# Kernel tuning notes

Hardware: AMD Instinct MI355X
Metric: run time of the kernel (lower is better)

Reference implementation:

```python
import jax, jax.numpy as jnp
import numpy as np

N_NODES = 50000
N_EDGES = 500000
IN_DIM = 128
HIDDEN = 32
HEADS = 8
OUT_DIM = HIDDEN * HEADS  # 256
NEG_SLOPE = 0.2


def setup_inputs() -> dict:
    key = jax.random.key(0)
    ks = jax.random.split(key, 10)
    s = lambda fan: 1.0 / np.sqrt(fan)
    x = jax.random.normal(ks[0], (N_NODES, IN_DIM), dtype=jnp.float32)
    edge_index = jax.random.randint(ks[1], (2, N_EDGES), 0, N_NODES, dtype=jnp.int32)
    W1 = jax.random.normal(ks[2], (IN_DIM, HEADS * HIDDEN), jnp.float32) * s(IN_DIM)
    a_src1 = jax.random.normal(ks[3], (HEADS, HIDDEN), jnp.float32) * s(HIDDEN)
    a_dst1 = jax.random.normal(ks[4], (HEADS, HIDDEN), jnp.float32) * s(HIDDEN)
    b1 = jnp.zeros((HEADS * HIDDEN,), jnp.float32)
    W2 = jax.random.normal(ks[5], (OUT_DIM, OUT_DIM), jnp.float32) * s(OUT_DIM)
    a_src2 = jax.random.normal(ks[6], (1, OUT_DIM), jnp.float32) * s(OUT_DIM)
    a_dst2 = jax.random.normal(ks[7], (1, OUT_DIM), jnp.float32) * s(OUT_DIM)
    b2 = jnp.zeros((OUT_DIM,), jnp.float32)
    return {"x": x, "edge_index": edge_index, "W1": W1, "a_src1": a_src1,
            "a_dst1": a_dst1, "b1": b1, "W2": W2, "a_src2": a_src2,
            "a_dst2": a_dst2, "b2": b2}


def _gat_layer(x, src, dst, W, a_src, a_dst, b, heads, ch, concat):
    N = x.shape[0]
    h = (x @ W).reshape(N, heads, ch)                      # [N,H,C]
    e_src = jnp.sum(h * a_src[None], axis=-1)              # [N,H]
    e_dst = jnp.sum(h * a_dst[None], axis=-1)              # [N,H]
    e = jax.nn.leaky_relu(e_src[src] + e_dst[dst], NEG_SLOPE)  # [E,H]
    # softmax over incoming edges of each destination node
    m = jax.ops.segment_max(e, dst, num_segments=N)        # [N,H]
    e = jnp.exp(e - m[dst])
    denom = jax.ops.segment_sum(e, dst, num_segments=N)    # [N,H]
    alpha = e / (denom[dst] + 1e-16)                       # [E,H]
    msg = h[src] * alpha[:, :, None]                       # [E,H,C]
    out = jax.ops.segment_sum(msg, dst, num_segments=N)    # [N,H,C]
    out = out.reshape(N, heads * ch) if concat else out.mean(axis=1)
    return out + b


def reference(x, edge_index, W1, a_src1, a_dst1, b1, W2, a_src2, a_dst2, b2):
    N = x.shape[0]
    # add self loops (PyG GATConv default)
    loops = jnp.arange(N, dtype=edge_index.dtype)
    src = jnp.concatenate([edge_index[0], loops])
    dst = jnp.concatenate([edge_index[1], loops])
    # dropout is identity in eval mode
    h = _gat_layer(x, src, dst, W1, a_src1, a_dst1, b1, HEADS, HIDDEN, True)
    h = jax.nn.elu(h)
    out = _gat_layer(h, src, dst, W2, a_src2, a_dst2, b2, 1, OUT_DIM, False)
    return out
```

## Files before the change

kernel.cpp:

```cpp
#include <hip/hip_runtime.h>
#include <math.h>

#define N_NODES 50000
#define E_ORIG  500000
#define E_TOT   550000
#define NB      196

typedef _Float16 half8 __attribute__((ext_vector_type(8)));
typedef _Float16 half4 __attribute__((ext_vector_type(4)));
typedef float    v4f   __attribute__((ext_vector_type(4)));

__global__ void k_prepw(const float* __restrict__ W1, const float* __restrict__ W2,
                        const float* __restrict__ as2, const float* __restrict__ ad2,
                        const int* __restrict__ ei,
                        _Float16* __restrict__ w1t, _Float16* __restrict__ w2t,
                        float* __restrict__ vs2, float* __restrict__ vd2,
                        int* __restrict__ deg) {
    int i = blockIdx.x * blockDim.x + threadIdx.x;
    if (i < E_TOT) {
        int d = (i < E_ORIG) ? ei[E_ORIG + i] : (i - E_ORIG);
        atomicAdd(&deg[d], 1);
        return;
    }
    int j = i - E_TOT;
    if (j < 128 * 256) {
        int k = j >> 8, c = j & 255;
        w1t[(size_t)c * 128 + k] = (_Float16)W1[j];
        return;
    }
    j -= 128 * 256;
    if (j < 256 * 256) {
        int k = j >> 8, c = j & 255;
        w2t[(size_t)c * 256 + k] = (_Float16)W2[j];
        return;
    }
    j -= 256 * 256;
    if (j < 256) {
        float s = 0.f, d = 0.f;
        for (int c = 0; c < 256; c++) {
            float w = W2[(size_t)j * 256 + c];
            s += w * as2[c];
            d += w * ad2[c];
        }
        vs2[j] = s;
        vd2[j] = d;
    }
}

__global__ __launch_bounds__(256) void k_blocksum(const int* __restrict__ deg,
                                                  int* __restrict__ bsum) {
    int t = threadIdx.x;
    int i = blockIdx.x * 256 + t;
    int v = (i < N_NODES) ? deg[i] : 0;
#pragma unroll
    for (int mk = 1; mk < 64; mk <<= 1) v += __shfl_xor(v, mk, 64);
    __shared__ int ws[4];
    if ((t & 63) == 0) ws[t >> 6] = v;
    __syncthreads();
    if (t == 0) bsum[blockIdx.x] = ws[0] + ws[1] + ws[2] + ws[3];
}

__global__ __launch_bounds__(256) void k_scanbsum(const int* __restrict__ bsum,
                                                  int* __restrict__ boff) {
    __shared__ int s[256];
    int t = threadIdx.x;
    int v = (t < NB) ? bsum[t] : 0;
    s[t] = v;
    __syncthreads();
    for (int o = 1; o < 256; o <<= 1) {
        int x = (t >= o) ? s[t - o] : 0;
        __syncthreads();
        s[t] += x;
        __syncthreads();
    }
    if (t <= NB) boff[t] = (t == 0) ? 0 : s[t - 1];
}

__global__ __launch_bounds__(256) void k_offsets(const int* __restrict__ deg,
                                                 const int* __restrict__ boff,
                                                 int* __restrict__ offsets,
                                                 int* __restrict__ cur) {
    __shared__ int s[256];
    int t = threadIdx.x;
    int i = blockIdx.x * 256 + t;
    int v = (i < N_NODES) ? deg[i] : 0;
    s[t] = v;
    __syncthreads();
    for (int o = 1; o < 256; o <<= 1) {
        int x = (t >= o) ? s[t - o] : 0;
        __syncthreads();
        s[t] += x;
        __syncthreads();
    }
    int off = boff[blockIdx.x] + s[t] - v;
    if (i <= N_NODES) {
        offsets[i] = off;
        if (i < N_NODES) cur[i] = off;
    }
}

__global__ void k_scatter(const int* __restrict__ ei, int* __restrict__ cur,
                          int* __restrict__ csr_src) {
    int e = blockIdx.x * blockDim.x + threadIdx.x;
    if (e >= E_TOT) return;
    int s, d;
    if (e < E_ORIG) { s = ei[e]; d = ei[E_ORIG + e]; }
    else            { s = e - E_ORIG; d = s; }
    int slot = atomicAdd(&cur[d], 1);
    csr_src[slot] = s;
}

__global__ __launch_bounds__(256) void k_gemm1(
    const float* __restrict__ X, const _Float16* __restrict__ Bt,
    const float* __restrict__ a_s, const float* __restrict__ a_d,
    _Float16* __restrict__ H, float* __restrict__ es, float* __restrict__ ed) {
    int t = threadIdx.x, w = t >> 6, lane = t & 63;
    int quad = lane >> 4, l16 = lane & 15;
    int row0 = blockIdx.x * 32;
    int colbase = w * 64;

    v4f acc[2][4];
#pragma unroll
    for (int i = 0; i < 2; i++)
#pragma unroll
        for (int j = 0; j < 4; j++) acc[i][j] = (v4f){0.f, 0.f, 0.f, 0.f};

    int r0 = row0 + l16;      if (r0 >= N_NODES) r0 = N_NODES - 1;
    int r1 = row0 + 16 + l16; if (r1 >= N_NODES) r1 = N_NODES - 1;
    const float4* a0p = (const float4*)(X + (size_t)r0 * 128) + quad * 2;
    const float4* a1p = (const float4*)(X + (size_t)r1 * 128) + quad * 2;
    const half8* bp[4];
#pragma unroll
    for (int ct = 0; ct < 4; ct++)
        bp[ct] = (const half8*)(Bt + (size_t)(colbase + ct * 16 + l16) * 128 + quad * 8);

#pragma unroll
    for (int kc = 0; kc < 4; kc++) {
        float4 f0 = a0p[kc * 8], f1 = a0p[kc * 8 + 1];
        float4 f2 = a1p[kc * 8], f3 = a1p[kc * 8 + 1];
        half8 av0 = (half8){(_Float16)f0.x, (_Float16)f0.y, (_Float16)f0.z, (_Float16)f0.w,
                            (_Float16)f1.x, (_Float16)f1.y, (_Float16)f1.z, (_Float16)f1.w};
        half8 av1 = (half8){(_Float16)f2.x, (_Float16)f2.y, (_Float16)f2.z, (_Float16)f2.w,
                            (_Float16)f3.x, (_Float16)f3.y, (_Float16)f3.z, (_Float16)f3.w};
#pragma unroll
        for (int ct = 0; ct < 4; ct++) {
            half8 bv = bp[ct][kc * 4];
            acc[0][ct] = __builtin_amdgcn_mfma_f32_16x16x32_f16(av0, bv, acc[0][ct], 0, 0, 0);
            acc[1][ct] = __builtin_amdgcn_mfma_f32_16x16x32_f16(av1, bv, acc[1][ct], 0, 0, 0);
        }
    }

    float asv[4], adv[4];
#pragma unroll
    for (int ct = 0; ct < 4; ct++) {
        asv[ct] = a_s[colbase + ct * 16 + l16];
        adv[ct] = a_d[colbase + ct * 16 + l16];
    }
#pragma unroll
    for (int rt = 0; rt < 2; rt++) {
#pragma unroll
        for (int hp = 0; hp < 2; hp++) {
#pragma unroll
            for (int reg = 0; reg < 4; reg++) {
                float ps = acc[rt][2 * hp][reg] * asv[2 * hp] +
                           acc[rt][2 * hp + 1][reg] * asv[2 * hp + 1];
                float pd = acc[rt][2 * hp][reg] * adv[2 * hp] +
                           acc[rt][2 * hp + 1][reg] * adv[2 * hp + 1];
#pragma unroll
                for (int mk = 1; mk < 16; mk <<= 1) {
                    ps += __shfl_xor(ps, mk, 64);
                    pd += __shfl_xor(pd, mk, 64);
                }
                if (l16 == 0) {
                    int row = row0 + rt * 16 + quad * 4 + reg;
                    if (row < N_NODES) {
                        int head = w * 2 + hp;
                        es[(size_t)row * 8 + head] = ps;
                        ed[(size_t)row * 8 + head] = pd;
                    }
                }
            }
        }
    }

    __shared__ _Float16 SH[16][264];
#pragma unroll
    for (int rt = 0; rt < 2; rt++) {
        if (rt) __syncthreads();
#pragma unroll
        for (int ct = 0; ct < 4; ct++)
#pragma unroll
            for (int reg = 0; reg < 4; reg++)
                SH[quad * 4 + reg][colbase + ct * 16 + l16] = (_Float16)acc[rt][ct][reg];
        __syncthreads();
#pragma unroll
        for (int j = 0; j < 2; j++) {
            int c = j * 256 + t;
            int row = c >> 5, col8 = c & 31;
            int gr = row0 + rt * 16 + row;
            if (gr < N_NODES)
                *(half8*)(H + (size_t)gr * 256 + col8 * 8) = *(const half8*)&SH[row][col8 * 8];
        }
    }
}

__global__ __launch_bounds__(256) void k_gemm2(
    const _Float16* __restrict__ A, const _Float16* __restrict__ Bt,
    const float* __restrict__ bias, float* __restrict__ OUT) {
    int t = threadIdx.x, w = t >> 6, lane = t & 63;
    int quad = lane >> 4, l16 = lane & 15;
    int row0 = blockIdx.x * 32;
    int colbase = w * 64;

    v4f acc[2][4];
#pragma unroll
    for (int i = 0; i < 2; i++)
#pragma unroll
        for (int j = 0; j < 4; j++) acc[i][j] = (v4f){0.f, 0.f, 0.f, 0.f};

    int r0 = row0 + l16;      if (r0 >= N_NODES) r0 = N_NODES - 1;
    int r1 = row0 + 16 + l16; if (r1 >= N_NODES) r1 = N_NODES - 1;
    const half8* a0 = (const half8*)(A + (size_t)r0 * 256 + quad * 8);
    const half8* a1 = (const half8*)(A + (size_t)r1 * 256 + quad * 8);
    const half8* bp[4];
#pragma unroll
    for (int ct = 0; ct < 4; ct++)
        bp[ct] = (const half8*)(Bt + (size_t)(colbase + ct * 16 + l16) * 256 + quad * 8);

#pragma unroll
    for (int kc = 0; kc < 8; kc++) {
        half8 av0 = a0[kc * 4];
        half8 av1 = a1[kc * 4];
#pragma unroll
        for (int ct = 0; ct < 4; ct++) {
            half8 bv = bp[ct][kc * 4];
            acc[0][ct] = __builtin_amdgcn_mfma_f32_16x16x32_f16(av0, bv, acc[0][ct], 0, 0, 0);
            acc[1][ct] = __builtin_amdgcn_mfma_f32_16x16x32_f16(av1, bv, acc[1][ct], 0, 0, 0);
        }
    }

    __shared__ float SF[16][260];
#pragma unroll
    for (int rt = 0; rt < 2; rt++) {
        if (rt) __syncthreads();
#pragma unroll
        for (int ct = 0; ct < 4; ct++)
#pragma unroll
            for (int reg = 0; reg < 4; reg++)
                SF[quad * 4 + reg][colbase + ct * 16 + l16] = acc[rt][ct][reg];
        __syncthreads();
#pragma unroll
        for (int j = 0; j < 4; j++) {
            int c = j * 256 + t;
            int row = c >> 6, c4 = c & 63;
            int gr = row0 + rt * 16 + row;
            if (gr < N_NODES) {
                float4 v = *(const float4*)&SF[row][c4 * 4];
                float4 bb = ((const float4*)bias)[c4];
                float4 o = make_float4(v.x + bb.x, v.y + bb.y, v.z + bb.z, v.w + bb.w);
                *(float4*)(OUT + (size_t)gr * 256 + c4 * 4) = o;
            }
        }
    }
}

__global__ __launch_bounds__(256) void k_agg1(
    const _Float16* __restrict__ H1, const float* __restrict__ es,
    const float* __restrict__ ed, const int* __restrict__ offsets,
    const int* __restrict__ csr_src, const float* __restrict__ b1,
    const float* __restrict__ vs2, const float* __restrict__ vd2,
    _Float16* __restrict__ out1, float* __restrict__ es2,
    float* __restrict__ ed2) {
    int t = threadIdx.x, w = t >> 6, lane = t & 63;
    int n = blockIdx.x * 4 + w;
    int hB = lane >> 3;
    int beg = offsets[n];
    int deg = offsets[n + 1] - beg;
    float edl = ed[(size_t)n * 8 + hB];

    const char* __restrict__ Hb  = (const char*)H1 + lane * 8;
    const char* __restrict__ esb = (const char*)es + hB * 4;
    float a0 = 0.f, a1 = 0.f, a2 = 0.f, a3 = 0.f, den = 0.f;

    for (int base = 0; base < deg; base += 64) {
        int rem = deg - base; if (rem > 64) rem = 64;
        int idx = beg + base + lane;
        if (idx >= E_TOT) idx = E_TOT - 1;
        int sreg = csr_src[idx];
        int i = 0;
        for (; i + 3 < rem; i += 4) {
            int s0 = __shfl(sreg, i), s1 = __shfl(sreg, i + 1);
            int s2 = __shfl(sreg, i + 2), s3 = __shfl(sreg, i + 3);
            float l0 = *(const float*)(esb + ((unsigned)s0 << 5)) + edl;
            float l1 = *(const float*)(esb + ((unsigned)s1 << 5)) + edl;
            float l2 = *(const float*)(esb + ((unsigned)s2 << 5)) + edl;
            float l3 = *(const float*)(esb + ((unsigned)s3 << 5)) + edl;
            half4 h0 = *(const half4*)(Hb + ((unsigned)s0 << 9));
            half4 h1 = *(const half4*)(Hb + ((unsigned)s1 << 9));
            half4 h2 = *(const half4*)(Hb + ((unsigned)s2 << 9));
            half4 h3 = *(const half4*)(Hb + ((unsigned)s3 << 9));
            l0 = l0 > 0.f ? l0 : 0.2f * l0;
            l1 = l1 > 0.f ? l1 : 0.2f * l1;
            l2 = l2 > 0.f ? l2 : 0.2f * l2;
            l3 = l3 > 0.f ? l3 : 0.2f * l3;
            float w0 = __expf(l0), w1 = __expf(l1);
            float w2 = __expf(l2), w3 = __expf(l3);
            a0 += w0 * (float)h0[0]; a1 += w0 * (float)h0[1];
            a2 += w0 * (float)h0[2]; a3 += w0 * (float)h0[3];
            a0 += w1 * (float)h1[0]; a1 += w1 * (float)h1[1];
            a2 += w1 * (float)h1[2]; a3 += w1 * (float)h1[3];
            a0 += w2 * (float)h2[0]; a1 += w2 * (float)h2[1];
            a2 += w2 * (float)h2[2]; a3 += w2 * (float)h2[3];
            a0 += w3 * (float)h3[0]; a1 += w3 * (float)h3[1];
            a2 += w3 * (float)h3[2]; a3 += w3 * (float)h3[3];
            den += w0 + w1 + w2 + w3;
        }
        for (; i < rem; i++) {
            int s0 = __shfl(sreg, i);
            float l0 = *(const float*)(esb + ((unsigned)s0 << 5)) + edl;
            l0 = l0 > 0.f ? l0 : 0.2f * l0;
            float w0 = __expf(l0);
            half4 h0 = *(const half4*)(Hb + ((unsigned)s0 << 9));
            a0 += w0 * (float)h0[0]; a1 += w0 * (float)h0[1];
            a2 += w0 * (float)h0[2]; a3 += w0 * (float)h0[3];
            den += w0;
        }
    }

    float r = 1.f / (den + 1e-16f);
    float4 bb = ((const float4*)b1)[lane];
    float o0 = a0 * r + bb.x, o1 = a1 * r + bb.y;
    float o2 = a2 * r + bb.z, o3 = a3 * r + bb.w;
    o0 = o0 > 0.f ? o0 : __expf(o0) - 1.f;
    o1 = o1 > 0.f ? o1 : __expf(o1) - 1.f;
    o2 = o2 > 0.f ? o2 : __expf(o2) - 1.f;
    o3 = o3 > 0.f ? o3 : __expf(o3) - 1.f;
    ((half4*)(out1 + (size_t)n * 256))[lane] =
        (half4){(_Float16)o0, (_Float16)o1, (_Float16)o2, (_Float16)o3};

    float4 vs = ((const float4*)vs2)[lane];
    float4 vd = ((const float4*)vd2)[lane];
    float ps = o0 * vs.x + o1 * vs.y + o2 * vs.z + o3 * vs.w;
    float pd = o0 * vd.x + o1 * vd.y + o2 * vd.z + o3 * vd.w;
#pragma unroll
    for (int mk = 1; mk < 64; mk <<= 1) {
        ps += __shfl_xor(ps, mk, 64);
        pd += __shfl_xor(pd, mk, 64);
    }
    if (lane == 0) { es2[n] = ps; ed2[n] = pd; }
}

__global__ __launch_bounds__(256) void k_agg2(
    const _Float16* __restrict__ O1, const float* __restrict__ es2,
    const float* __restrict__ ed2, const int* __restrict__ offsets,
    const int* __restrict__ csr_src, _Float16* __restrict__ xagg) {
    int t = threadIdx.x, w = t >> 6, lane = t & 63;
    int n = blockIdx.x * 4 + w;
    int beg = offsets[n];
    int deg = offsets[n + 1] - beg;
    float edn = ed2[n];

    const char* __restrict__ Ob  = (const char*)O1 + lane * 8;
    const char* __restrict__ eb  = (const char*)es2;
    float a0 = 0.f, a1 = 0.f, a2 = 0.f, a3 = 0.f, den = 0.f;

    for (int base = 0; base < deg; base += 64) {
        int rem = deg - base; if (rem > 64) rem = 64;
        int idx = beg + base + lane;
        if (idx >= E_TOT) idx = E_TOT - 1;
        int sreg = csr_src[idx];
        int i = 0;
        for (; i + 3 < rem; i += 4) {
            int s0 = __shfl(sreg, i), s1 = __shfl(sreg, i + 1);
            int s2 = __shfl(sreg, i + 2), s3 = __shfl(sreg, i + 3);
            float l0 = *(const float*)(eb + ((unsigned)s0 << 2)) + edn;
            float l1 = *(const float*)(eb + ((unsigned)s1 << 2)) + edn;
            float l2 = *(const float*)(eb + ((unsigned)s2 << 2)) + edn;
            float l3 = *(const float*)(eb + ((unsigned)s3 << 2)) + edn;
            half4 h0 = *(const half4*)(Ob + ((unsigned)s0 << 9));
            half4 h1 = *(const half4*)(Ob + ((unsigned)s1 << 9));
            half4 h2 = *(const half4*)(Ob + ((unsigned)s2 << 9));
            half4 h3 = *(const half4*)(Ob + ((unsigned)s3 << 9));
            l0 = l0 > 0.f ? l0 : 0.2f * l0;
            l1 = l1 > 0.f ? l1 : 0.2f * l1;
            l2 = l2 > 0.f ? l2 : 0.2f * l2;
            l3 = l3 > 0.f ? l3 : 0.2f * l3;
            float w0 = __expf(l0), w1 = __expf(l1);
            float w2 = __expf(l2), w3 = __expf(l3);
            a0 += w0 * (float)h0[0]; a1 += w0 * (float)h0[1];
            a2 += w0 * (float)h0[2]; a3 += w0 * (float)h0[3];
            a0 += w1 * (float)h1[0]; a1 += w1 * (float)h1[1];
            a2 += w1 * (float)h1[2]; a3 += w1 * (float)h1[3];
            a0 += w2 * (float)h2[0]; a1 += w2 * (float)h2[1];
            a2 += w2 * (float)h2[2]; a3 += w2 * (float)h2[3];
            a0 += w3 * (float)h3[0]; a1 += w3 * (float)h3[1];
            a2 += w3 * (float)h3[2]; a3 += w3 * (float)h3[3];
            den += w0 + w1 + w2 + w3;
        }
        for (; i < rem; i++) {
            int s0 = __shfl(sreg, i);
            float l0 = *(const float*)(eb + ((unsigned)s0 << 2)) + edn;
            l0 = l0 > 0.f ? l0 : 0.2f * l0;
            float w0 = __expf(l0);
            half4 h0 = *(const half4*)(Ob + ((unsigned)s0 << 9));
            a0 += w0 * (float)h0[0]; a1 += w0 * (float)h0[1];
            a2 += w0 * (float)h0[2]; a3 += w0 * (float)h0[3];
            den += w0;
        }
    }

    float r = 1.f / (den + 1e-16f);
    ((half4*)(xagg + (size_t)n * 256))[lane] =
        (half4){(_Float16)(a0 * r), (_Float16)(a1 * r),
                (_Float16)(a2 * r), (_Float16)(a3 * r)};
}

extern "C" void kernel_launch(void* const* d_in, const int* in_sizes, int n_in,
                              void* d_out, int out_size, void* d_ws, size_t ws_size,
                              hipStream_t stream) {
    const float* x   = (const float*)d_in[0];
    const int*   ei  = (const int*)d_in[1];
    const float* W1  = (const float*)d_in[2];
    const float* as1 = (const float*)d_in[3];
    const float* ad1 = (const float*)d_in[4];
    const float* b1  = (const float*)d_in[5];
    const float* W2  = (const float*)d_in[6];
    const float* as2 = (const float*)d_in[7];
    const float* ad2 = (const float*)d_in[8];
    const float* b2  = (const float*)d_in[9];
    float* out = (float*)d_out;

    char* ws = (char*)d_ws;
    size_t off = 0;
    auto alloc = [&](size_t bytes) {
        void* p = ws + off;
        off = (off + bytes + 255) & ~(size_t)255;
        return p;
    };
    _Float16* h1h     = (_Float16*)alloc((size_t)N_NODES * 256 * 2);
    _Float16* out1h   = (_Float16*)alloc((size_t)N_NODES * 256 * 2);
    _Float16* xagg    = (_Float16*)alloc((size_t)N_NODES * 256 * 2);
    _Float16* w1t     = (_Float16*)alloc((size_t)128 * 256 * 2);
    _Float16* w2t     = (_Float16*)alloc((size_t)256 * 256 * 2);
    float*    es1     = (float*)alloc((size_t)N_NODES * 8 * 4);
    float*    ed1     = (float*)alloc((size_t)N_NODES * 8 * 4);
    float*    es2     = (float*)alloc((size_t)N_NODES * 4);
    float*    ed2     = (float*)alloc((size_t)N_NODES * 4);
    float*    vs2     = (float*)alloc(256 * 4);
    float*    vd2     = (float*)alloc(256 * 4);
    int*      deg     = (int*)alloc((size_t)N_NODES * 4);
    int*      offsets = (int*)alloc((size_t)(N_NODES + 1) * 4);
    int*      cur     = (int*)alloc((size_t)N_NODES * 4);
    int*      csr_src = (int*)alloc((size_t)E_TOT * 4);
    int*      bsum    = (int*)alloc((size_t)NB * 4);
    int*      boff    = (int*)alloc((size_t)(NB + 1) * 4);

    const int TB = 256;
    int gridE = (E_TOT + TB - 1) / TB;
    int gridG = (N_NODES + 31) / 32;
    int gridA = N_NODES / 4;

    hipMemsetAsync(deg, 0, (size_t)N_NODES * 4, stream);
    int prepN = E_TOT + 128 * 256 + 256 * 256 + 256;
    k_prepw<<<(prepN + TB - 1) / TB, TB, 0, stream>>>(W1, W2, as2, ad2, ei,
                                                      w1t, w2t, vs2, vd2, deg);
    k_blocksum<<<NB, TB, 0, stream>>>(deg, bsum);
    k_scanbsum<<<1, TB, 0, stream>>>(bsum, boff);
    k_offsets<<<NB, TB, 0, stream>>>(deg, boff, offsets, cur);
    k_scatter<<<gridE, TB, 0, stream>>>(ei, cur, csr_src);

    k_gemm1<<<gridG, TB, 0, stream>>>(x, w1t, as1, ad1, h1h, es1, ed1);
    k_agg1<<<gridA, TB, 0, stream>>>(h1h, es1, ed1, offsets, csr_src, b1,
                                     vs2, vd2, out1h, es2, ed2);

    k_agg2<<<gridA, TB, 0, stream>>>(out1h, es2, ed2, offsets, csr_src, xagg);
    k_gemm2<<<gridG, TB, 0, stream>>>(xagg, w2t, b2, out);
}
```

Before: 318.9 us.

## Compute attention weights once per edge chunk and broadcast via readlane

In both aggregation kernels, each lane now computes the attention logit and exp for one edge of the 64-edge chunk up front, instead of every lane recomputing it for every edge. Layer 1 writes the per-head weights to a shared-memory table and layer 2 broadcasts them with readlane, which removes redundant gathers of es and duplicate exp work. The inner loop is unrolled by 8 and uses scalar readlane in place of shfl for source indices. The layer-1 path relies on a manual lgkmcnt wait rather than a barrier, which is safe only because each wave touches its own slice of the table.

```diff
diff --git a/kernel.cpp b/kernel.cpp
--- a/kernel.cpp
+++ b/kernel.cpp
@@ -264,6 +264,14 @@
     }
 }
 
+#define EDGE1(I) {                                                         \
+    unsigned su = (unsigned)__builtin_amdgcn_readlane(sreg, (I));          \
+    float wb = wrow[(I)];                                                  \
+    half4 hv = *((const half4*)((const char*)H1 + ((size_t)su << 9)) + lane); \
+    a0 += wb * (float)hv[0]; a1 += wb * (float)hv[1];                      \
+    a2 += wb * (float)hv[2]; a3 += wb * (float)hv[3];                      \
+    den += wb; }
+
 __global__ __launch_bounds__(256) void k_agg1(
     const _Float16* __restrict__ H1, const float* __restrict__ es,
     const float* __restrict__ ed, const int* __restrict__ offsets,
@@ -276,10 +284,18 @@
     int hB = lane >> 3;
     int beg = offsets[n];
     int deg = offsets[n + 1] - beg;
-    float edl = ed[(size_t)n * 8 + hB];
-
-    const char* __restrict__ Hb  = (const char*)H1 + lane * 8;
-    const char* __restrict__ esb = (const char*)es + hB * 4;
+
+    float edv[8];
+    {
+        const float4* edp = (const float4*)(ed + (size_t)n * 8);
+        float4 d0 = edp[0], d1 = edp[1];
+        edv[0] = d0.x; edv[1] = d0.y; edv[2] = d0.z; edv[3] = d0.w;
+        edv[4] = d1.x; edv[5] = d1.y; edv[6] = d1.z; edv[7] = d1.w;
+    }
+
+    __shared__ float WT[4][8][68];
+    float* wrow = &WT[w][hB][0];
+
     float a0 = 0.f, a1 = 0.f, a2 = 0.f, a3 = 0.f, den = 0.f;
 
     for (int base = 0; base < deg; base += 64) {
@@ -287,44 +303,33 @@
         int idx = beg + base + lane;
         if (idx >= E_TOT) idx = E_TOT - 1;
         int sreg = csr_src[idx];
-        int i = 0;
-        for (; i + 3 < rem; i += 4) {
-            int s0 = __shfl(sreg, i), s1 = __shfl(sreg, i + 1);
-            int s2 = __shfl(sreg, i + 2), s3 = __shfl(sreg, i + 3);
-            float l0 = *(const float*)(esb + ((unsigned)s0 << 5)) + edl;
-            float l1 = *(const float*)(esb + ((unsigned)s1 << 5)) + edl;
-            float l2 = *(const float*)(esb + ((unsigned)s2 << 5)) + edl;
-            float l3 = *(const float*)(esb + ((unsigned)s3 << 5)) + edl;
-            half4 h0 = *(const half4*)(Hb + ((unsigned)s0 << 9));
-            half4 h1 = *(const half4*)(Hb + ((unsigned)s1 << 9));
-            half4 h2 = *(const half4*)(Hb + ((unsigned)s2 << 9));
-            half4 h3 = *(const half4*)(Hb + ((unsigned)s3 << 9));
-            l0 = l0 > 0.f ? l0 : 0.2f * l0;
-            l1 = l1 > 0.f ? l1 : 0.2f * l1;
-            l2 = l2 > 0.f ? l2 : 0.2f * l2;
-            l3 = l3 > 0.f ? l3 : 0.2f * l3;
-            float w0 = __expf(l0), w1 = __expf(l1);
-            float w2 = __expf(l2), w3 = __expf(l3);
-            a0 += w0 * (float)h0[0]; a1 += w0 * (float)h0[1];
-            a2 += w0 * (float)h0[2]; a3 += w0 * (float)h0[3];
-            a0 += w1 * (float)h1[0]; a1 += w1 * (float)h1[1];
-            a2 += w1 * (float)h1[2]; a3 += w1 * (float)h1[3];
-            a0 += w2 * (float)h2[0]; a1 += w2 * (float)h2[1];
-            a2 += w2 * (float)h2[2]; a3 += w2 * (float)h2[3];
-            a0 += w3 * (float)h3[0]; a1 += w3 * (float)h3[1];
-            a2 += w3 * (float)h3[2]; a3 += w3 * (float)h3[3];
-            den += w0 + w1 + w2 + w3;
-        }
-        for (; i < rem; i++) {
-            int s0 = __shfl(sreg, i);
-            float l0 = *(const float*)(esb + ((unsigned)s0 << 5)) + edl;
-            l0 = l0 > 0.f ? l0 : 0.2f * l0;
-            float w0 = __expf(l0);
-            half4 h0 = *(const half4*)(Hb + ((unsigned)s0 << 9));
-            a0 += w0 * (float)h0[0]; a1 += w0 * (float)h0[1];
-            a2 += w0 * (float)h0[2]; a3 += w0 * (float)h0[3];
-            den += w0;
-        }
+
+        {
+            const float4* ep = (const float4*)(es + ((size_t)(unsigned)sreg << 3));
+            float4 e0 = ep[0], e1 = ep[1];
+            float l0 = e0.x + edv[0], l1 = e0.y + edv[1];
+            float l2 = e0.z + edv[2], l3 = e0.w + edv[3];
+            float l4 = e1.x + edv[4], l5 = e1.y + edv[5];
+            float l6 = e1.z + edv[6], l7 = e1.w + edv[7];
+            l0 = fmaxf(l0, 0.2f * l0); l1 = fmaxf(l1, 0.2f * l1);
+            l2 = fmaxf(l2, 0.2f * l2); l3 = fmaxf(l3, 0.2f * l3);
+            l4 = fmaxf(l4, 0.2f * l4); l5 = fmaxf(l5, 0.2f * l5);
+            l6 = fmaxf(l6, 0.2f * l6); l7 = fmaxf(l7, 0.2f * l7);
+            WT[w][0][lane] = __expf(l0); WT[w][1][lane] = __expf(l1);
+            WT[w][2][lane] = __expf(l2); WT[w][3][lane] = __expf(l3);
+            WT[w][4][lane] = __expf(l4); WT[w][5][lane] = __expf(l5);
+            WT[w][6][lane] = __expf(l6); WT[w][7][lane] = __expf(l7);
+        }
+        asm volatile("s_waitcnt lgkmcnt(0)" ::: "memory");
+
+        int i = 0, nf = rem & ~7;
+        for (; i < nf; i += 8) {
+            EDGE1(i);     EDGE1(i + 1); EDGE1(i + 2); EDGE1(i + 3);
+            EDGE1(i + 4); EDGE1(i + 5); EDGE1(i + 6); EDGE1(i + 7);
+        }
+        if (rem & 4) { EDGE1(i); EDGE1(i + 1); EDGE1(i + 2); EDGE1(i + 3); i += 4; }
+        if (rem & 2) { EDGE1(i); EDGE1(i + 1); i += 2; }
+        if (rem & 1) { EDGE1(i); }
     }
 
     float r = 1.f / (den + 1e-16f);
@@ -350,6 +355,14 @@
     if (lane == 0) { es2[n] = ps; ed2[n] = pd; }
 }
 
+#define EDGE2(I) {                                                         \
+    unsigned su = (unsigned)__builtin_amdgcn_readlane(sreg, (I));          \
+    float wb = __int_as_float(__builtin_amdgcn_readlane(wbits, (I)));      \
+    half4 hv = *((const half4*)((const char*)O1 + ((size_t)su << 9)) + lane); \
+    a0 += wb * (float)hv[0]; a1 += wb * (float)hv[1];                      \
+    a2 += wb * (float)hv[2]; a3 += wb * (float)hv[3];                      \
+    den += wb; }
+
 __global__ __launch_bounds__(256) void k_agg2(
     const _Float16* __restrict__ O1, const float* __restrict__ es2,
     const float* __restrict__ ed2, const int* __restrict__ offsets,
@@ -360,8 +373,6 @@
     int deg = offsets[n + 1] - beg;
     float edn = ed2[n];
 
-    const char* __restrict__ Ob  = (const char*)O1 + lane * 8;
-    const char* __restrict__ eb  = (const char*)es2;
     float a0 = 0.f, a1 = 0.f, a2 = 0.f, a3 = 0.f, den = 0.f;
 
     for (int base = 0; base < deg; base += 64) {
@@ -369,44 +380,19 @@
         int idx = beg + base + lane;
         if (idx >= E_TOT) idx = E_TOT - 1;
         int sreg = csr_src[idx];
-        int i = 0;
-        for (; i + 3 < rem; i += 4) {
-            int s0 = __shfl(sreg, i), s1 = __shfl(sreg, i + 1);
-            int s2 = __shfl(sreg, i + 2), s3 = __shfl(sreg, i + 3);
-            float l0 = *(const float*)(eb + ((unsigned)s0 << 2)) + edn;
-            float l1 = *(const float*)(eb + ((unsigned)s1 << 2)) + edn;
-            float l2 = *(const float*)(eb + ((unsigned)s2 << 2)) + edn;
-            float l3 = *(const float*)(eb + ((unsigned)s3 << 2)) + edn;
-            half4 h0 = *(const half4*)(Ob + ((unsigned)s0 << 9));
-            half4 h1 = *(const half4*)(Ob + ((unsigned)s1 << 9));
-            half4 h2 = *(const half4*)(Ob + ((unsigned)s2 << 9));
-            half4 h3 = *(const half4*)(Ob + ((unsigned)s3 << 9));
-            l0 = l0 > 0.f ? l0 : 0.2f * l0;
-            l1 = l1 > 0.f ? l1 : 0.2f * l1;
-            l2 = l2 > 0.f ? l2 : 0.2f * l2;
-            l3 = l3 > 0.f ? l3 : 0.2f * l3;
-            float w0 = __expf(l0), w1 = __expf(l1);
-            float w2 = __expf(l2), w3 = __expf(l3);
-            a0 += w0 * (float)h0[0]; a1 += w0 * (float)h0[1];
-            a2 += w0 * (float)h0[2]; a3 += w0 * (float)h0[3];
-            a0 += w1 * (float)h1[0]; a1 += w1 * (float)h1[1];
-            a2 += w1 * (float)h1[2]; a3 += w1 * (float)h1[3];
-            a0 += w2 * (float)h2[0]; a1 += w2 * (float)h2[1];
-            a2 += w2 * (float)h2[2]; a3 += w2 * (float)h2[3];
-            a0 += w3 * (float)h3[0]; a1 += w3 * (float)h3[1];
-            a2 += w3 * (float)h3[2]; a3 += w3 * (float)h3[3];
-            den += w0 + w1 + w2 + w3;
-        }
-        for (; i < rem; i++) {
-            int s0 = __shfl(sreg, i);
-            float l0 = *(const float*)(eb + ((unsigned)s0 << 2)) + edn;
-            l0 = l0 > 0.f ? l0 : 0.2f * l0;
-            float w0 = __expf(l0);
-            half4 h0 = *(const half4*)(Ob + ((unsigned)s0 << 9));
-            a0 += w0 * (float)h0[0]; a1 += w0 * (float)h0[1];
-            a2 += w0 * (float)h0[2]; a3 += w0 * (float)h0[3];
-            den += w0;
-        }
+
+        float l = es2[sreg] + edn;
+        l = fmaxf(l, 0.2f * l);
+        int wbits = __float_as_int(__expf(l));
+
+        int i = 0, nf = rem & ~7;
+        for (; i < nf; i += 8) {
+            EDGE2(i);     EDGE2(i + 1); EDGE2(i + 2); EDGE2(i + 3);
+            EDGE2(i + 4); EDGE2(i + 5); EDGE2(i + 6); EDGE2(i + 7);
+        }
+        if (rem & 4) { EDGE2(i); EDGE2(i + 1); EDGE2(i + 2); EDGE2(i + 3); i += 4; }
+        if (rem & 2) { EDGE2(i); EDGE2(i + 1); i += 2; }
+        if (rem & 1) { EDGE2(i); }
     }
 
     float r = 1.f / (den + 1e-16f);
```

Result: slower. 327.8 us (+2.8%).
